# Optimization experiments

Measured on AMD Instinct MI355X. Metric: run time of the kernel, lower is better.

## Reference

```python
import jax, jax.numpy as jnp
import numpy as np

B, T, D = 2, 2048, 1024
H = 16
HD = D // H
WINDOW = 128
N_GLOBAL = 1
SCALE = 1.0 / np.sqrt(HD)


def _attend_mask(T):
    # True = allowed to attend: banded local window + global rows/cols
    idx = jnp.arange(T)
    dist = jnp.abs(idx[:, None] - idx[None, :])
    attend = dist <= WINDOW
    glb = idx < N_GLOBAL
    attend = attend | glb[:, None] | glb[None, :]
    return attend  # [T, T] bool


def setup_inputs() -> dict:
    key = jax.random.key(0)
    ks = jax.random.split(key, 5)
    scale_w = 1.0 / np.sqrt(D)
    return {
        "x": jax.random.normal(ks[0], (B, T, D), dtype=jnp.float32),
        "Wq": jax.random.normal(ks[1], (D, D), dtype=jnp.float32) * scale_w,
        "Wk": jax.random.normal(ks[2], (D, D), dtype=jnp.float32) * scale_w,
        "Wv": jax.random.normal(ks[3], (D, D), dtype=jnp.float32) * scale_w,
        "Wo": jax.random.normal(ks[4], (D, D), dtype=jnp.float32) * scale_w,
    }


def reference(x, Wq, Wk, Wv, Wo):
    Bb, Tt, Dd = x.shape
    # torch nn.Linear: y = x @ W.T
    q = (x @ Wq.T).reshape(Bb, Tt, H, HD).transpose(0, 2, 1, 3)  # [B,H,T,hd]
    k = (x @ Wk.T).reshape(Bb, Tt, H, HD).transpose(0, 2, 1, 3)
    v = (x @ Wv.T).reshape(Bb, Tt, H, HD).transpose(0, 2, 1, 3)

    attend = _attend_mask(Tt)  # [T,T]
    logits = jnp.einsum("bhqd,bhkd->bhqk", q, k) * SCALE
    logits = jnp.where(attend[None, None, :, :], logits, -jnp.inf)
    weights = jax.nn.softmax(logits, axis=-1)
    weights = jnp.nan_to_num(weights)
    out = jnp.einsum("bhqk,bhkd->bhqd", weights, v)
    out = out.transpose(0, 2, 1, 3).reshape(Bb, Tt, Dd)
    return out @ Wo.T
```

## Files before the change

### kernel.cpp

```cpp
#include <hip/hip_runtime.h>

typedef unsigned short u16;
typedef __attribute__((ext_vector_type(8))) __bf16 bf16x8;
typedef __attribute__((ext_vector_type(4))) float f32x4;
typedef __attribute__((ext_vector_type(8))) u16 u16x8;
typedef __attribute__((ext_vector_type(4))) u16 u16x4;

#define T_SEQ 2048
#define DIM   1024
#define HDIM  64
#define WIN   128
#define XN_EL (2 * T_SEQ * DIM)

#define AS1 __attribute__((address_space(1)))
#define AS3 __attribute__((address_space(3)))

__device__ __forceinline__ u16 f2bf(float f) {
  union { float f; unsigned u; } v; v.f = f;
  unsigned r = v.u + 0x7fffu + ((v.u >> 16) & 1u);
  return (u16)(r >> 16);
}
__device__ __forceinline__ float bf2f(u16 u) {
  union { unsigned u; float f; } v; v.u = ((unsigned)u) << 16; return v.f;
}
__device__ __forceinline__ void bar() {
  asm volatile("" ::: "memory");
  __builtin_amdgcn_s_barrier();
  asm volatile("" ::: "memory");
}

__global__ __launch_bounds__(256) void cvt_all(
    const float* __restrict__ x,  const float* __restrict__ wq,
    const float* __restrict__ wk, const float* __restrict__ wv,
    const float* __restrict__ wo, u16* __restrict__ xb, u16* __restrict__ wb) {
  const int bid = blockIdx.x;
  const float* s;
  u16* d;
  int off;
  if (bid < 2048) {
    s = x; d = xb; off = bid * 2048;
  } else {
    const int w = bid - 2048;
    const int m = w >> 9;
    s = (m == 0) ? wq : ((m == 1) ? wk : ((m == 2) ? wv : wo));
    d = wb + ((size_t)m << 20);
    off = (w & 511) * 2048;
  }
  const int i = off + threadIdx.x * 8;
  const float4* s4 = (const float4*)(s + i);
  float4 a = s4[0], b = s4[1];
  u16x8 r;
  r[0] = f2bf(a.x); r[1] = f2bf(a.y); r[2] = f2bf(a.z); r[3] = f2bf(a.w);
  r[4] = f2bf(b.x); r[5] = f2bf(b.y); r[6] = f2bf(b.z); r[7] = f2bf(b.w);
  *(u16x8*)(d + i) = r;
}

template <int BM, int BN, int WM, int WN, int OS, int SPLIT, typename OUT_T>
__global__ __launch_bounds__(WM * WN * 64, 2) void gemm3(
    const u16* __restrict__ A, const u16* __restrict__ B,
    OUT_T* __restrict__ C, int nbm) {
  constexpr int NW = WM * WN;
  constexpr int RM = BM / WM, RN = BN / WN;
  constexpr int MF = RM / 16, NF = RN / 16;
  constexpr int MPH = MF / 4;
  constexpr int NT = DIM / 64;
  constexpr int CA = BM / 8, CB = BN / 8;
  constexpr int ANW = CA / NW;
  constexpr int BNW = CB / NW;

  __shared__ u16 As[2][BM * 64];
  __shared__ u16 Bs[2][BN * 64];

  const int tid = threadIdx.x;
  const int lane = tid & 63;
  const int wid = tid >> 6;
  const int wr = wid / WN, wc = wid % WN;
  const int c15 = lane & 15, g = lane >> 4;
  const int lr = lane >> 3;
  const int lcs = ((lane & 7) ^ lr) << 3;

  const int cpx = gridDim.x >> 3;
  const int bid = ((int)blockIdx.x & 7) * cpx + ((int)blockIdx.x >> 3);
  const int bm = bid % nbm;
  const int nb = bid / nbm;
  const u16* Ab = A + (size_t)bm * BM * DIM;
  const u16* Bb = B + (size_t)nb * BN * DIM;

  f32x4 acc[MF][NF];
#pragma unroll
  for (int m = 0; m < MF; ++m)
#pragma unroll
    for (int n = 0; n < NF; ++n) acc[m][n] = (f32x4){0.f, 0.f, 0.f, 0.f};

  auto stA = [&](int buf, int half, int k0) {
#pragma unroll
    for (int i = 0; i < ANW / 2; ++i) {
      const int c = half * (CA / 2) + wid * (ANW / 2) + i;
      __builtin_amdgcn_global_load_lds(
          (const AS1 void*)(Ab + (size_t)(c * 8 + lr) * DIM + k0 + lcs),
          (AS3 void*)(&As[buf][c * 512]), 16, 0, 0);
    }
  };
  auto stB = [&](int buf, int k0) {
#pragma unroll
    for (int i = 0; i < BNW; ++i) {
      const int c = wid * BNW + i;
      __builtin_amdgcn_global_load_lds(
          (const AS1 void*)(Bb + (size_t)(c * 8 + lr) * DIM + k0 + lcs),
          (AS3 void*)(&Bs[buf][c * 512]), 16, 0, 0);
    }
  };

  stA(0, 0, 0); stA(0, 1, 0);
  stB(0, 0); stB(1, 64);
  if constexpr (BNW == 3) asm volatile("s_waitcnt vmcnt(3)" ::: "memory");
  else                    asm volatile("s_waitcnt vmcnt(4)" ::: "memory");
  bar();

  for (int t = 0; t < NT; ++t) {
    const int buf = t & 1;
    const int k0 = t * 64;
    bf16x8 bfrag[NF][2];
#pragma unroll
    for (int p = 0; p < 4; ++p) {
      if (p == 0) {
#pragma unroll
        for (int n = 0; n < NF; ++n)
#pragma unroll
          for (int ks = 0; ks < 2; ++ks) {
            const int r = wc * RN + n * 16 + c15;
            bfrag[n][ks] = *(const bf16x8*)(
                &Bs[buf][r * 64 + ((ks * 32 + g * 8) ^ ((r & 7) << 3))]);
          }
      }
      bf16x8 af[MPH][2];
#pragma unroll
      for (int m = 0; m < MPH; ++m)
#pragma unroll
        for (int ks = 0; ks < 2; ++ks) {
          const int r = wr * RM + (p * MPH + m) * 16 + c15;
          af[m][ks] = *(const bf16x8*)(
              &As[buf][r * 64 + ((ks * 32 + g * 8) ^ ((r & 7) << 3))]);
        }
      if (p == 0) {
        if (t + 1 < NT) stA(buf ^ 1, 0, k0 + 64);
      } else if (p == 1) {
        if (t + 1 < NT) stA(buf ^ 1, 1, k0 + 64);
      } else if (p == 2) {
        if (t + 2 < NT) stB(buf, k0 + 128);
      } else {
        if (t < NT - 2) {
          if constexpr (BNW == 3) asm volatile("s_waitcnt vmcnt(3)" ::: "memory");
          else                    asm volatile("s_waitcnt vmcnt(4)" ::: "memory");
        } else {
          asm volatile("s_waitcnt vmcnt(0)" ::: "memory");
        }
      }
      bar();
      __builtin_amdgcn_s_setprio(1);
#pragma unroll
      for (int m = 0; m < MPH; ++m)
#pragma unroll
        for (int n = 0; n < NF; ++n)
#pragma unroll
          for (int ks = 0; ks < 2; ++ks)
            acc[p * MPH + m][n] = __builtin_amdgcn_mfma_f32_16x16x32_bf16(
                af[m][ks], bfrag[n][ks], acc[p * MPH + m][n], 0, 0, 0);
      __builtin_amdgcn_s_setprio(0);
      bar();
    }
  }

#pragma unroll
  for (int m = 0; m < MF; ++m) {
    const int row0 = bm * BM + wr * RM + m * 16 + g * 4;
#pragma unroll
    for (int n = 0; n < NF; ++n) {
      const int col = nb * BN + wc * RN + n * 16 + c15;
      if constexpr (SPLIT) {
        if (col < 2048) {
#pragma unroll
          for (int j = 0; j < 4; ++j) {
            u16* dst = (u16*)C + (size_t)(col >> 10) * (size_t)XN_EL +
                       (col & 1023) + (size_t)(row0 + j) * DIM;
            *dst = f2bf(acc[m][n][j]);
          }
        } else {
          const int h = (col - 2048) >> 6, dd = (col - 2048) & 63;
          u16x4 pk;
#pragma unroll
          for (int j = 0; j < 4; ++j) pk[j] = f2bf(acc[m][n][j]);
          const size_t vidx =
              ((size_t)((row0 >> 11) * 16 + h) * 64 + dd) * T_SEQ + (row0 & 2047);
          *(u16x4*)((u16*)C + (size_t)2 * XN_EL + vidx) = pk;
        }
      } else {
#pragma unroll
        for (int j = 0; j < 4; ++j) {
          const size_t idx = (size_t)(row0 + j) * OS + col;
          if constexpr (sizeof(OUT_T) == 2) C[idx] = f2bf(acc[m][n][j]);
          else C[idx] = acc[m][n][j];
        }
      }
    }
  }
}

__global__ __launch_bounds__(256) void sparse_attn(
    const u16* __restrict__ Q, const u16* __restrict__ K,
    const u16* __restrict__ VT, u16* __restrict__ AO) {
  __shared__ u16 Kt[2][64 * 64];
  __shared__ u16 Vt[2][64 * 64];
  __shared__ u16 Pl[4][16 * 72];
  __shared__ float Pg[4][16];

  const int tid = threadIdx.x;
  const int lane = tid & 63;
  const int wid = tid >> 6;
  const size_t ha = (size_t)blockIdx.z * T_SEQ * DIM + (size_t)blockIdx.y * HDIM;
  const size_t hv = ((size_t)blockIdx.z * 16 + blockIdx.y) * HDIM * T_SEQ;
  const u16* Qp = Q + ha;
  const u16* Kp = K + ha;
  const u16* Vp = VT + hv;

  if (blockIdx.x == 32) {
    float* qs   = (float*)Pl;
    float* ps   = (float*)(&Kt[0][0]);
    float* rbuf = (float*)(&Vt[0][0]);
    float* red  = (float*)Pg;

    if (tid < HDIM) qs[tid] = bf2f(Qp[tid]);
    __syncthreads();

    float lsum = 0.f;
#pragma unroll
    for (int j = 0; j < 8; ++j) {
      const int k = tid + 256 * j;
      const u16* kr = Kp + (size_t)k * DIM;
      float acc = 0.f;
#pragma unroll
      for (int d0 = 0; d0 < 8; ++d0) {
        u16x8 kv = *(const u16x8*)(kr + d0 * 8);
#pragma unroll
        for (int e = 0; e < 8; ++e) acc += qs[d0 * 8 + e] * bf2f(kv[e]);
      }
      const float p = __expf(acc * 0.125f);
      ps[k] = p;
      lsum += p;
    }
#pragma unroll
    for (int s = 1; s < 64; s <<= 1) lsum += __shfl_xor(lsum, s);
    if (lane == 0) red[wid] = lsum;
    __syncthreads();
    const float denom = red[0] + red[1] + red[2] + red[3];

    const int d = tid & 63, kc = tid >> 6;
    const u16* vr = Vp + (size_t)d * T_SEQ + kc * 512;
    float facc = 0.f;
#pragma unroll 4
    for (int i = 0; i < 512; i += 8) {
      const u16x8 vv = *(const u16x8*)(vr + i);
#pragma unroll
      for (int e = 0; e < 8; ++e) facc += ps[kc * 512 + i + e] * bf2f(vv[e]);
    }
    rbuf[kc * 64 + d] = facc;
    __syncthreads();
    if (tid < HDIM) {
      const float tot = rbuf[tid] + rbuf[64 + tid] + rbuf[128 + tid] + rbuf[192 + tid];
      AO[ha + tid] = f2bf(tot / denom);
    }
    return;
  }

  const int c15 = lane & 15;
  const int g = lane >> 4;
  const int q0 = blockIdx.x * 64;

  bf16x8 qf0, qf1;
  {
    const u16* qp = Qp + (size_t)(q0 + wid * 16 + c15) * DIM + g * 8;
    qf0 = *(const bf16x8*)qp;
    qf1 = *(const bf16x8*)(qp + 32);
  }

  float lrun[4] = {0.f, 0.f, 0.f, 0.f};
  f32x4 ao[4];
#pragma unroll
  for (int c = 0; c < 4; ++c) ao[c] = (f32x4){0.f, 0.f, 0.f, 0.f};

  const int klo = (q0 > WIN) ? (q0 - WIN) : 0;
  int khi = q0 + 64 + WIN;
  if (khi > T_SEQ) khi = T_SEQ;
  const int nt = (khi - klo) >> 6;

  const int lr = lane >> 3;
  const int lcs = ((lane & 7) ^ lr) << 3;

  auto stage = [&](int buf, int kt) {
#pragma unroll
    for (int i = 0; i < 2; ++i) {
      const int c = wid * 2 + i;
      __builtin_amdgcn_global_load_lds(
          (const AS1 void*)(Kp + (size_t)(kt + c * 8 + lr) * DIM + lcs),
          (AS3 void*)(&Kt[buf][c * 512]), 16, 0, 0);
      __builtin_amdgcn_global_load_lds(
          (const AS1 void*)(Vp + (size_t)(c * 8 + lr) * T_SEQ + kt + lcs),
          (AS3 void*)(&Vt[buf][c * 512]), 16, 0, 0);
    }
  };

  stage(0, klo);
  asm volatile("s_waitcnt vmcnt(0)" ::: "memory");
  __syncthreads();

  for (int ti = 0; ti < nt; ++ti) {
    const int kt = klo + ti * 64;
    const int buf = ti & 1;
    if (ti + 1 < nt) stage(buf ^ 1, kt + 64);

    f32x4 s[4];
#pragma unroll
    for (int t = 0; t < 4; ++t) {
      const int r = t * 16 + c15;
      bf16x8 ka = *(const bf16x8*)(&Kt[buf][r * 64 + ((g * 8) ^ ((r & 7) << 3))]);
      bf16x8 kb = *(const bf16x8*)(&Kt[buf][r * 64 + ((32 + g * 8) ^ ((r & 7) << 3))]);
      s[t] = (f32x4){0.f, 0.f, 0.f, 0.f};
      s[t] = __builtin_amdgcn_mfma_f32_16x16x32_bf16(qf0, ka, s[t], 0, 0, 0);
      s[t] = __builtin_amdgcn_mfma_f32_16x16x32_bf16(qf1, kb, s[t], 0, 0, 0);
    }
    if (kt >= q0 - 65 && kt <= q0 + 65) {
#pragma unroll
      for (int j = 0; j < 4; ++j) {
#pragma unroll
        for (int t = 0; t < 4; ++t) {
          const float p = __expf(s[t][j] * 0.125f);
          lrun[j] += p;
          Pl[wid][(g * 4 + j) * 72 + t * 16 + c15] = f2bf(p);
        }
      }
    } else {
#pragma unroll
      for (int j = 0; j < 4; ++j) {
        const int qg = q0 + wid * 16 + g * 4 + j;
#pragma unroll
        for (int t = 0; t < 4; ++t) {
          const int kg = kt + t * 16 + c15;
          const int dd = qg - kg;
          const bool ok = (kg == 0) || (dd <= WIN && dd >= -WIN);
          const float p = ok ? __expf(s[t][j] * 0.125f) : 0.f;
          lrun[j] += p;
          Pl[wid][(g * 4 + j) * 72 + t * 16 + c15] = f2bf(p);
        }
      }
    }
    asm volatile("s_waitcnt lgkmcnt(0)" ::: "memory");

    const bf16x8 pa0 = *(const bf16x8*)(&Pl[wid][c15 * 72 + g * 8]);
    const bf16x8 pa1 = *(const bf16x8*)(&Pl[wid][c15 * 72 + 32 + g * 8]);
#pragma unroll
    for (int c = 0; c < 4; ++c) {
      const int r = c * 16 + c15;
      bf16x8 va = *(const bf16x8*)(&Vt[buf][r * 64 + ((g * 8) ^ ((r & 7) << 3))]);
      bf16x8 vb = *(const bf16x8*)(&Vt[buf][r * 64 + ((32 + g * 8) ^ ((r & 7) << 3))]);
      ao[c] = __builtin_amdgcn_mfma_f32_16x16x32_bf16(pa0, va, ao[c], 0, 0, 0);
      ao[c] = __builtin_amdgcn_mfma_f32_16x16x32_bf16(pa1, vb, ao[c], 0, 0, 0);
    }
    __syncthreads();
  }

  float ltot[4];
#pragma unroll
  for (int j = 0; j < 4; ++j) {
    float ls = lrun[j];
    ls += __shfl_xor(ls, 1);
    ls += __shfl_xor(ls, 2);
    ls += __shfl_xor(ls, 4);
    ls += __shfl_xor(ls, 8);
    ltot[j] = ls;
  }

  if (klo > 0) {
    const u16x8 qu0 = *(const u16x8*)&qf0;
    const u16x8 qu1 = *(const u16x8*)&qf1;
    const u16x8 k0a = *(const u16x8*)(Kp + g * 8);
    const u16x8 k0b = *(const u16x8*)(Kp + 32 + g * 8);
    float sg = 0.f;
#pragma unroll
    for (int e = 0; e < 8; ++e)
      sg += bf2f(qu0[e]) * bf2f(k0a[e]) + bf2f(qu1[e]) * bf2f(k0b[e]);
    sg += __shfl_xor(sg, 16);
    sg += __shfl_xor(sg, 32);
    const float pg = __expf(sg * 0.125f);
    Pg[wid][c15] = pg;
    asm volatile("s_waitcnt lgkmcnt(0)" ::: "memory");
#pragma unroll
    for (int j = 0; j < 4; ++j) {
      const float pj = Pg[wid][g * 4 + j];
      ltot[j] += pj;
#pragma unroll
      for (int c = 0; c < 4; ++c)
        ao[c][j] += pj * bf2f(Vp[(size_t)(c * 16 + c15) * T_SEQ]);
    }
  }

#pragma unroll
  for (int j = 0; j < 4; ++j) {
    const int qrow = q0 + wid * 16 + g * 4 + j;
    if (qrow == 0) continue;
    const float inv = 1.0f / ltot[j];
#pragma unroll
    for (int c = 0; c < 4; ++c)
      AO[ha + (size_t)qrow * DIM + c * 16 + c15] = f2bf(ao[c][j] * inv);
  }
}

extern "C" void kernel_launch(void* const* d_in, const int* in_sizes, int n_in,
                              void* d_out, int out_size, void* d_ws, size_t ws_size,
                              hipStream_t stream) {
  const float* x  = (const float*)d_in[0];
  const float* Wq = (const float*)d_in[1];
  const float* Wk = (const float*)d_in[2];
  const float* Wv = (const float*)d_in[3];
  const float* Wo = (const float*)d_in[4];
  float* out = (float*)d_out;

  const int WN = DIM * DIM;

  u16* ws  = (u16*)d_ws;
  u16* xb  = ws;
  u16* wb  = ws + (size_t)XN_EL;
  u16* Wob = wb + (size_t)3 * WN;
  u16* Qb  = wb + (size_t)4 * WN;
  u16* Kb  = Qb + (size_t)XN_EL;
  u16* VTb = Qb + (size_t)2 * XN_EL;

  cvt_all<<<4096, 256, 0, stream>>>(x, Wq, Wk, Wv, Wo, xb, wb);

  gemm3<256, 192, 2, 4, DIM, 1, u16><<<256, 512, 0, stream>>>(xb, wb, Qb, 16);

  sparse_attn<<<dim3(33, 16, 2), 256, 0, stream>>>(Qb, Kb, VTb, xb);

  gemm3<128, 128, 2, 2, DIM, 0, float><<<256, 256, 0, stream>>>(xb, Wob, out, 32);
}
```

Baseline: 114.7 us.

## Load K/V fragments directly from global memory instead of LDS double-buffering

```diff
diff --git a/kernel.cpp b/kernel.cpp
--- a/kernel.cpp
+++ b/kernel.cpp
@@ -209,10 +209,9 @@
 __global__ __launch_bounds__(256) void sparse_attn(
     const u16* __restrict__ Q, const u16* __restrict__ K,
     const u16* __restrict__ VT, u16* __restrict__ AO) {
-  __shared__ u16 Kt[2][64 * 64];
-  __shared__ u16 Vt[2][64 * 64];
   __shared__ u16 Pl[4][16 * 72];
   __shared__ float Pg[4][16];
+  __shared__ float Gaux[328];
 
   const int tid = threadIdx.x;
   const int lane = tid & 63;
@@ -224,9 +223,9 @@
   const u16* Vp = VT + hv;
 
   if (blockIdx.x == 32) {
-    float* qs   = (float*)Pl;
-    float* ps   = (float*)(&Kt[0][0]);
-    float* rbuf = (float*)(&Vt[0][0]);
+    float* qs   = Gaux;
+    float* rbuf = Gaux + 64;
+    float* ps   = (float*)(&Pl[0][0]);
     float* red  = (float*)Pg;
 
     if (tid < HDIM) qs[tid] = bf2f(Qp[tid]);
@@ -293,41 +292,20 @@
   if (khi > T_SEQ) khi = T_SEQ;
   const int nt = (khi - klo) >> 6;
 
-  const int lr = lane >> 3;
-  const int lcs = ((lane & 7) ^ lr) << 3;
-
-  auto stage = [&](int buf, int kt) {
-#pragma unroll
-    for (int i = 0; i < 2; ++i) {
-      const int c = wid * 2 + i;
-      __builtin_amdgcn_global_load_lds(
-          (const AS1 void*)(Kp + (size_t)(kt + c * 8 + lr) * DIM + lcs),
-          (AS3 void*)(&Kt[buf][c * 512]), 16, 0, 0);
-      __builtin_amdgcn_global_load_lds(
-          (const AS1 void*)(Vp + (size_t)(c * 8 + lr) * T_SEQ + kt + lcs),
-          (AS3 void*)(&Vt[buf][c * 512]), 16, 0, 0);
-    }
-  };
-
-  stage(0, klo);
-  asm volatile("s_waitcnt vmcnt(0)" ::: "memory");
-  __syncthreads();
-
   for (int ti = 0; ti < nt; ++ti) {
     const int kt = klo + ti * 64;
-    const int buf = ti & 1;
-    if (ti + 1 < nt) stage(buf ^ 1, kt + 64);
 
     f32x4 s[4];
 #pragma unroll
     for (int t = 0; t < 4; ++t) {
-      const int r = t * 16 + c15;
-      bf16x8 ka = *(const bf16x8*)(&Kt[buf][r * 64 + ((g * 8) ^ ((r & 7) << 3))]);
-      bf16x8 kb = *(const bf16x8*)(&Kt[buf][r * 64 + ((32 + g * 8) ^ ((r & 7) << 3))]);
-      s[t] = (f32x4){0.f, 0.f, 0.f, 0.f};
-      s[t] = __builtin_amdgcn_mfma_f32_16x16x32_bf16(qf0, ka, s[t], 0, 0, 0);
-      s[t] = __builtin_amdgcn_mfma_f32_16x16x32_bf16(qf1, kb, s[t], 0, 0, 0);
-    }
+      const u16* kr = Kp + (size_t)(kt + t * 16 + c15) * DIM + g * 8;
+      const bf16x8 ka = *(const bf16x8*)kr;
+      const bf16x8 kb = *(const bf16x8*)(kr + 32);
+      f32x4 z = (f32x4){0.f, 0.f, 0.f, 0.f};
+      z = __builtin_amdgcn_mfma_f32_16x16x32_bf16(qf0, ka, z, 0, 0, 0);
+      s[t] = __builtin_amdgcn_mfma_f32_16x16x32_bf16(qf1, kb, z, 0, 0, 0);
+    }
+
     if (kt >= q0 - 65 && kt <= q0 + 65) {
 #pragma unroll
       for (int j = 0; j < 4; ++j) {
@@ -359,13 +337,12 @@
     const bf16x8 pa1 = *(const bf16x8*)(&Pl[wid][c15 * 72 + 32 + g * 8]);
 #pragma unroll
     for (int c = 0; c < 4; ++c) {
-      const int r = c * 16 + c15;
-      bf16x8 va = *(const bf16x8*)(&Vt[buf][r * 64 + ((g * 8) ^ ((r & 7) << 3))]);
-      bf16x8 vb = *(const bf16x8*)(&Vt[buf][r * 64 + ((32 + g * 8) ^ ((r & 7) << 3))]);
+      const u16* vr = Vp + (size_t)(c * 16 + c15) * T_SEQ + kt + g * 8;
+      const bf16x8 va = *(const bf16x8*)vr;
+      const bf16x8 vb = *(const bf16x8*)(vr + 32);
       ao[c] = __builtin_amdgcn_mfma_f32_16x16x32_bf16(pa0, va, ao[c], 0, 0, 0);
       ao[c] = __builtin_amdgcn_mfma_f32_16x16x32_bf16(pa1, vb, ao[c], 0, 0, 0);
     }
-    __syncthreads();
   }
 
   float ltot[4];
```

New measurement: 132.7 us. +15.7%, slower.
